# Kernel tuning notes

Measured on AMD Instinct MI355X. Metric: run time of the kernel, lower is better.

The kernel has to match this reference:

```python
import jax, jax.numpy as jnp
import numpy as np

D_EMB = 128
N_CLASSES = 10
ITEM_DIM = 64


def _mlp(x, w1, b1, w2, b2):
    # torch nn.GELU default is exact (erf) gelu
    return jax.nn.gelu(x @ w1 + b1, approximate=False) @ w2 + b2


def sparsemax(z, axis=-1):
    """Euclidean projection of logits onto the probability simplex (sparsemax)."""
    n = z.shape[axis]
    z_sorted = -jnp.sort(-z, axis=axis)                      # descending
    ks = jnp.arange(1, n + 1, dtype=z.dtype)
    csum = jnp.cumsum(z_sorted, axis=axis)
    support = (1.0 + ks * z_sorted) > csum                   # broadcast over last axis
    k_z = jnp.sum(support, axis=axis, keepdims=True)         # support size
    csum_k = jnp.take_along_axis(csum, k_z.astype(jnp.int32) - 1, axis=axis)
    tau = (csum_k - 1.0) / k_z.astype(z.dtype)
    return jnp.maximum(z - tau, 0.0)


def setup_inputs() -> dict:
    key = jax.random.key(0)
    ks = jax.random.split(key, 22)
    d = D_EMB

    def lin(k, fan_in, fan_out):
        lim = (1.0 / fan_in) ** 0.5
        kw, kb = jax.random.split(k)
        w = jax.random.uniform(kw, (fan_in, fan_out), jnp.float32, -lim, lim)
        b = jax.random.uniform(kb, (fan_out,), jnp.float32, -lim, lim)
        return w, b

    wx1, bx1 = lin(ks[0], ITEM_DIM, d)
    wx2, bx2 = lin(ks[1], d, d)
    wq1, bq1 = lin(ks[2], 1, d)
    wq2, bq2 = lin(ks[3], d, d)
    wqp, bqp = lin(ks[4], d, d)
    wkp, bkp = lin(ks[5], d, d)
    wvp, bvp = lin(ks[6], d, d)
    wp1, bp1 = lin(ks[7], d, d)
    wp2, bp2 = lin(ks[8], d, N_CLASSES)

    x_items = jax.random.normal(ks[9], (32, 16384, ITEM_DIM), jnp.float32)
    x_query = jax.random.normal(ks[10], (32, 1), jnp.float32)
    return {
        "x_items": x_items, "x_query": x_query,
        "wx1": wx1, "bx1": bx1, "wx2": wx2, "bx2": bx2,
        "wq1": wq1, "bq1": bq1, "wq2": wq2, "bq2": bq2,
        "wqp": wqp, "bqp": bqp, "wkp": wkp, "bkp": bkp,
        "wvp": wvp, "bvp": bvp, "wp1": wp1, "bp1": bp1,
        "wp2": wp2, "bp2": bp2,
    }


def reference(x_items, x_query, wx1, bx1, wx2, bx2, wq1, bq1, wq2, bq2,
              wqp, bqp, wkp, bkp, wvp, bvp, wp1, bp1, wp2, bp2):
    # x_items: [B, N, item_dim]; x_query: [B, 1] -> unsqueeze(-1) -> [B, 1, 1]
    h_items = _mlp(x_items, wx1, bx1, wx2, bx2)              # [B, N, d]
    h_query = _mlp(x_query[..., None], wq1, bq1, wq2, bq2)   # [B, 1, d]
    q = h_query @ wqp + bqp                                   # [B, 1, d]
    k = h_items @ wkp + bkp                                   # [B, N, d]
    v = h_items @ wvp + bvp                                   # [B, N, d]
    scale = k.shape[-1] ** -0.5
    scores = jnp.einsum('bqd,bnd->bqn', q, k) * scale         # [B, 1, N]
    attn = sparsemax(scores, axis=-1)                         # simplex mapping
    z = jnp.einsum('bqn,bnd->bqd', attn, v)[:, 0]             # squeeze(1) -> [B, d]
    return _mlp(z, wp1, bp1, wp2, bp2)                        # [B, n_classes]
```

## Files before the change

### kernel.cpp

```cpp
#include <hip/hip_runtime.h>
#include <hip/hip_bf16.h>
#include <cstdint>

#define BATCH 32
#define NITEMS 16384
#define DEMB 128
#define IDIM 64

typedef short short8 __attribute__((ext_vector_type(8)));
typedef float f32x4 __attribute__((ext_vector_type(4)));

__device__ inline unsigned short f2bf(float f) {
    union { float f; unsigned int u; } v; v.f = f;
    unsigned int u = v.u;
    unsigned int r = (u + 0x7FFFu + ((u >> 16) & 1u)) >> 16;
    return (unsigned short)r;
}
__device__ inline float bf2f(unsigned short h) {
    union { unsigned int u; float f; } v; v.u = ((unsigned int)h) << 16;
    return v.f;
}

__device__ inline float gelu_f(float x) {
    float y = fabsf(x) * 0.70710678118654752f;
    float t = __builtin_amdgcn_rcpf(fmaf(0.3275911f, y, 1.0f));
    float p = fmaf(0.5307027145f, t, -0.7265760135f);
    p = fmaf(p, t, 0.7107068705f);
    p = fmaf(p, t, -0.142248368f);
    p = fmaf(p, t, 0.127414796f);
    p = p * t;
    float e = __builtin_amdgcn_exp2f(x * x * -0.72134752044448171f);
    float q = p * e;
    float phi = (x > 0.f) ? (1.0f - q) : q;
    return x * phi;
}

__global__ __launch_bounds__(128) void k0_prep(
    const float* __restrict__ xq, const float* __restrict__ wq1, const float* __restrict__ bq1,
    const float* __restrict__ wq2, const float* __restrict__ bq2,
    const float* __restrict__ wqp, const float* __restrict__ bqp,
    const float* __restrict__ wkp,
    const float* __restrict__ wx1, const float* __restrict__ wx2,
    float* __restrict__ r_out, unsigned short* __restrict__ w1h, unsigned short* __restrict__ w1l) {
    __shared__ float buf1[128], buf2[128], buf3[128], buf4[128];
    int t = threadIdx.x;
    int blk = blockIdx.x;
    if (blk < BATCH) {
        int b = blk;
        float xqv = xq[b];
        buf1[t] = gelu_f(fmaf(xqv, wq1[t], bq1[t]));
        __syncthreads();
        float acc = bq2[t];
        for (int j = 0; j < 128; j++) acc = fmaf(buf1[j], wq2[j * 128 + t], acc);
        buf2[t] = acc;
        __syncthreads();
        acc = bqp[t];
        for (int j = 0; j < 128; j++) acc = fmaf(buf2[j], wqp[j * 128 + t], acc);
        buf3[t] = acc;
        __syncthreads();
        acc = 0.f;
        for (int i = 0; i < 128; i++) acc = fmaf(wkp[t * 128 + i], buf3[i], acc);
        buf4[t] = acc * 0.08838834764831845f;
        __syncthreads();
        acc = 0.f;
        for (int i = 0; i < 128; i++) acc = fmaf(wx2[t * 128 + i], buf4[i], acc);
        r_out[b * 128 + t] = acc;
    } else {
        for (int idx = t; idx < 64 * 128; idx += 128) {
            int k = idx >> 7, n = idx & 127;
            float v = wx1[idx];
            unsigned short hi = f2bf(v);
            float lo = v - bf2f(hi);
            w1h[n * 64 + k] = hi;
            w1l[n * 64 + k] = f2bf(lo);
        }
    }
}

__global__ __launch_bounds__(256) void k1_items(
    const float* __restrict__ x, const unsigned short* __restrict__ w1h,
    const unsigned short* __restrict__ w1l, const float* __restrict__ bx1,
    const float* __restrict__ r_in, float* __restrict__ scores) {
    __shared__ alignas(16) unsigned short lxh[64 * 72];
    __shared__ alignas(16) unsigned short lxl[64 * 72];
    __shared__ float red[4][64];
    int tid = threadIdx.x;
    int wave = tid >> 6, lane = tid & 63;
    int quad = lane >> 4, l15 = lane & 15;
    int tile = blockIdx.x;
    long item0 = (long)tile * 64;
    int b = tile >> 8;

    short8 wh[2][2], wl[2][2];
    for (int s = 0; s < 2; s++)
        for (int mt = 0; mt < 2; mt++) {
            int off = (wave * 32 + mt * 16 + l15) * 64 + s * 32 + quad * 8;
            wh[s][mt] = *(const short8*)(w1h + off);
            wl[s][mt] = *(const short8*)(w1l + off);
        }
    float bias8[2][4], rv8[2][4];
    for (int mt = 0; mt < 2; mt++)
        for (int rr = 0; rr < 4; rr++) {
            int row = wave * 32 + mt * 16 + quad * 4 + rr;
            bias8[mt][rr] = bx1[row];
            rv8[mt][rr] = r_in[b * 128 + row];
        }

    const float* xg = x + item0 * 64;
    for (int p = 0; p < 4; p++) {
        int idx = tid + p * 256;
        int row = idx >> 4, c4 = (idx & 15) * 4;
        float4 v = *(const float4*)(xg + row * 64 + c4);
        unsigned int ux = __float_as_uint(v.x), uy = __float_as_uint(v.y);
        unsigned int uz = __float_as_uint(v.z), uw = __float_as_uint(v.w);
        unsigned int hi01 = __builtin_amdgcn_perm(uy, ux, 0x07060302u);
        unsigned int hi23 = __builtin_amdgcn_perm(uw, uz, 0x07060302u);
        float lx = v.x - __uint_as_float(ux & 0xFFFF0000u);
        float ly = v.y - __uint_as_float(uy & 0xFFFF0000u);
        float lz = v.z - __uint_as_float(uz & 0xFFFF0000u);
        float lw = v.w - __uint_as_float(uw & 0xFFFF0000u);
        unsigned int lo01 = __builtin_amdgcn_perm(__float_as_uint(ly), __float_as_uint(lx), 0x07060302u);
        unsigned int lo23 = __builtin_amdgcn_perm(__float_as_uint(lw), __float_as_uint(lz), 0x07060302u);
        *(uint2*)(lxh + row * 72 + c4) = make_uint2(hi01, hi23);
        *(uint2*)(lxl + row * 72 + c4) = make_uint2(lo01, lo23);
    }
    __syncthreads();

    f32x4 acc[2][4];
    for (int mt = 0; mt < 2; mt++)
        for (int nt = 0; nt < 4; nt++) {
            f32x4 bi = {bias8[mt][0], bias8[mt][1], bias8[mt][2], bias8[mt][3]};
            acc[mt][nt] = bi;
        }

    for (int s = 0; s < 2; s++) {
        int koff = s * 32 + quad * 8;
        short8 xh[4], xl[4];
        for (int nt = 0; nt < 4; nt++) {
            int rb = (nt * 16 + l15) * 72 + koff;
            xh[nt] = *(const short8*)(lxh + rb);
            xl[nt] = *(const short8*)(lxl + rb);
        }
        for (int mt = 0; mt < 2; mt++)
            for (int nt = 0; nt < 4; nt++) {
                acc[mt][nt] = __builtin_amdgcn_mfma_f32_16x16x32_bf16(wh[s][mt], xl[nt], acc[mt][nt], 0, 0, 0);
                acc[mt][nt] = __builtin_amdgcn_mfma_f32_16x16x32_bf16(wl[s][mt], xh[nt], acc[mt][nt], 0, 0, 0);
                acc[mt][nt] = __builtin_amdgcn_mfma_f32_16x16x32_bf16(wh[s][mt], xh[nt], acc[mt][nt], 0, 0, 0);
            }
    }

    float pr[4] = {0.f, 0.f, 0.f, 0.f};
    for (int mt = 0; mt < 2; mt++)
        for (int nt = 0; nt < 4; nt++)
            for (int rr = 0; rr < 4; rr++) {
                float g = gelu_f(acc[mt][nt][rr]);
                pr[nt] = fmaf(g, rv8[mt][rr], pr[nt]);
            }
    for (int nt = 0; nt < 4; nt++) {
        pr[nt] += __shfl_xor(pr[nt], 16);
        pr[nt] += __shfl_xor(pr[nt], 32);
    }
    if (quad == 0)
        for (int nt = 0; nt < 4; nt++)
            red[wave][nt * 16 + l15] = pr[nt];
    __syncthreads();
    if (tid < 64)
        scores[item0 + tid] = red[0][tid] + red[1][tid] + red[2][tid] + red[3][tid];
}

__global__ __launch_bounds__(1024) void k2_tau(const float* __restrict__ scores,
                                               float* __restrict__ tau_out,
                                               float* __restrict__ u) {
    __shared__ float la[2][16], lc[2][16];
    int b = blockIdx.x, t = threadIdx.x;
    int wid = t >> 6, lane = t & 63;
    const float* s = scores + (size_t)b * NITEMS;
    float z[16];
    for (int i = 0; i < 16; i++) z[i] = s[t + i * 1024];
    float sm = 0.f;
    for (int i = 0; i < 16; i++) sm += z[i];
    for (int off = 32; off; off >>= 1) sm += __shfl_xor(sm, off);
    if (lane == 0) la[1][wid] = sm;
    __syncthreads();
    float tot = 0.f;
    for (int i = 0; i < 16; i++) tot += la[1][i];
    float tau = (tot - 1.0f) * (1.0f / 16384.0f);
    for (int it = 0; it < 20; it++) {
        int pb = it & 1;
        float ls = 0.f, ct = 0.f;
        for (int i = 0; i < 16; i++) {
            bool a = z[i] > tau;
            ls += a ? z[i] : 0.f;
            ct += a ? 1.f : 0.f;
        }
        for (int off = 32; off; off >>= 1) {
            ls += __shfl_xor(ls, off);
            ct += __shfl_xor(ct, off);
        }
        if (lane == 0) { la[pb][wid] = ls; lc[pb][wid] = ct; }
        __syncthreads();
        float tls = 0.f, tct = 0.f;
        for (int i = 0; i < 16; i++) { tls += la[pb][i]; tct += lc[pb][i]; }
        tau = (tls - 1.0f) / tct;
    }
    if (t == 0) tau_out[b] = tau;
    if (t < 128) u[b * 128 + t] = 0.f;
}

__global__ __launch_bounds__(256) void k3_support(
    const float* __restrict__ scores, const float* __restrict__ tau_in,
    const float* __restrict__ x,
    const float* __restrict__ wx1, const float* __restrict__ bx1,
    const float* __restrict__ wx2, const float* __restrict__ bx2,
    float* __restrict__ u) {
    __shared__ float red[4][128];
    int blk = blockIdx.x;
    int b = blk >> 5;
    int sub = blk & 31;
    int wave = threadIdx.x >> 6, lane = threadIdx.x & 63;
    int wslot = sub * 4 + wave;
    int base = wslot * 128;
    float tau = tau_in[b];
    int t0 = lane, t1 = lane + 64;
    float bb0 = bx1[t0], bb1 = bx1[t1];
    float cc0 = bx2[t0], cc1 = bx2[t1];
    float u0 = 0.f, u1 = 0.f;
    const float* srow = scores + (size_t)b * NITEMS + base;
    for (int half = 0; half < 2; half++) {
        float sv = srow[half * 64 + lane] - tau;
        unsigned long long mask = __ballot(sv > 0.f);
        while (mask) {
            int src = __ffsll((long long)mask) - 1;
            mask &= mask - 1;
            float wgt = __shfl(sv, src);
            int item = base + half * 64 + src;
            const float* xr = x + ((size_t)b * NITEMS + item) * 64;
            float xv = xr[lane];
            float p0 = bb0, p1 = bb1;
            for (int k = 0; k < 64; k++) {
                float xk = __shfl(xv, k);
                p0 = fmaf(xk, wx1[k * 128 + t0], p0);
                p1 = fmaf(xk, wx1[k * 128 + t1], p1);
            }
            float h0 = gelu_f(p0), h1 = gelu_f(p1);
            float a0 = cc0, a1 = cc1;
            for (int j = 0; j < 64; j++) {
                float hj = __shfl(h0, j);
                a0 = fmaf(hj, wx2[j * 128 + t0], a0);
                a1 = fmaf(hj, wx2[j * 128 + t1], a1);
            }
            for (int j = 0; j < 64; j++) {
                float hj = __shfl(h1, j);
                a0 = fmaf(hj, wx2[(j + 64) * 128 + t0], a0);
                a1 = fmaf(hj, wx2[(j + 64) * 128 + t1], a1);
            }
            u0 = fmaf(wgt, a0, u0);
            u1 = fmaf(wgt, a1, u1);
        }
    }
    red[wave][t0] = u0;
    red[wave][t1] = u1;
    __syncthreads();
    if (threadIdx.x < 128) {
        float s = red[0][threadIdx.x] + red[1][threadIdx.x] +
                  red[2][threadIdx.x] + red[3][threadIdx.x];
        atomicAdd(&u[b * 128 + threadIdx.x], s);
    }
}

__global__ __launch_bounds__(128) void k4_head(
    const float* __restrict__ u, const float* __restrict__ wvp, const float* __restrict__ bvp,
    const float* __restrict__ wp1, const float* __restrict__ bp1,
    const float* __restrict__ wp2, const float* __restrict__ bp2,
    float* __restrict__ out) {
    __shared__ float ub[128], zb[128], tb[128];
    int b = blockIdx.x, t = threadIdx.x;
    ub[t] = u[b * 128 + t];
    __syncthreads();
    float z = bvp[t];
    for (int j = 0; j < 128; j++) z = fmaf(ub[j], wvp[j * 128 + t], z);
    zb[t] = z;
    __syncthreads();
    float h = bp1[t];
    for (int j = 0; j < 128; j++) h = fmaf(zb[j], wp1[j * 128 + t], h);
    tb[t] = gelu_f(h);
    __syncthreads();
    if (t < 10) {
        float o = bp2[t];
        for (int j = 0; j < 128; j++) o = fmaf(tb[j], wp2[j * 10 + t], o);
        out[b * 10 + t] = o;
    }
}

extern "C" void kernel_launch(void* const* d_in, const int* in_sizes, int n_in,
                              void* d_out, int out_size, void* d_ws, size_t ws_size,
                              hipStream_t stream) {
    const float* x_items = (const float*)d_in[0];
    const float* x_query = (const float*)d_in[1];
    const float* wx1 = (const float*)d_in[2];
    const float* bx1 = (const float*)d_in[3];
    const float* wx2 = (const float*)d_in[4];
    const float* bx2 = (const float*)d_in[5];
    const float* wq1 = (const float*)d_in[6];
    const float* bq1 = (const float*)d_in[7];
    const float* wq2 = (const float*)d_in[8];
    const float* bq2 = (const float*)d_in[9];
    const float* wqp = (const float*)d_in[10];
    const float* bqp = (const float*)d_in[11];
    const float* wkp = (const float*)d_in[12];
    const float* wvp = (const float*)d_in[14];
    const float* bvp = (const float*)d_in[15];
    const float* wp1 = (const float*)d_in[16];
    const float* bp1 = (const float*)d_in[17];
    const float* wp2 = (const float*)d_in[18];
    const float* bp2 = (const float*)d_in[19];
    float* out = (float*)d_out;

    char* ws = (char*)d_ws;
    float* r_buf        = (float*)(ws);
    unsigned short* w1h = (unsigned short*)(ws + 16384);
    unsigned short* w1l = (unsigned short*)(ws + 32768);
    float* scores       = (float*)(ws + 49152);
    float* tau          = (float*)(ws + 49152 + 2097152);
    float* u            = (float*)(ws + 49152 + 2097152 + 256);

    k0_prep<<<33, 128, 0, stream>>>(x_query, wq1, bq1, wq2, bq2, wqp, bqp, wkp,
                                    wx1, wx2, r_buf, w1h, w1l);
    k1_items<<<(BATCH * NITEMS) / 64, 256, 0, stream>>>(x_items, w1h, w1l, bx1, r_buf, scores);
    k2_tau<<<BATCH, 1024, 0, stream>>>(scores, tau, u);
    k3_support<<<BATCH * 32, 256, 0, stream>>>(scores, tau, x_items, wx1, bx1, wx2, bx2, u);
    k4_head<<<BATCH, 128, 0, stream>>>(u, wvp, bvp, wp1, bp1, wp2, bp2, out);
}
```

Baseline: 329.6 us.

## Fuse head MLP into support kernel via last-block counter; early-exit tau iteration

The head kernel is folded into the support kernel. Each batch has a per-batch atomic counter, and the last of its 32 blocks to finish computes the value projection and output MLP, which removes one kernel launch. The tau fixed-point iteration now starts from a very low threshold and exits as soon as tau stops changing, replacing the fixed 20 iterations and the initial mean pass. This adds fences, an extra atomic and a data-dependent loop bound, and starting from a lower tau may need more iterations to converge.

```diff
diff --git a/kernel.cpp b/kernel.cpp
--- a/kernel.cpp
+++ b/kernel.cpp
@@ -170,22 +170,16 @@
 
 __global__ __launch_bounds__(1024) void k2_tau(const float* __restrict__ scores,
                                                float* __restrict__ tau_out,
-                                               float* __restrict__ u) {
+                                               float* __restrict__ u,
+                                               int* __restrict__ ctr) {
     __shared__ float la[2][16], lc[2][16];
     int b = blockIdx.x, t = threadIdx.x;
     int wid = t >> 6, lane = t & 63;
     const float* s = scores + (size_t)b * NITEMS;
     float z[16];
     for (int i = 0; i < 16; i++) z[i] = s[t + i * 1024];
-    float sm = 0.f;
-    for (int i = 0; i < 16; i++) sm += z[i];
-    for (int off = 32; off; off >>= 1) sm += __shfl_xor(sm, off);
-    if (lane == 0) la[1][wid] = sm;
-    __syncthreads();
-    float tot = 0.f;
-    for (int i = 0; i < 16; i++) tot += la[1][i];
-    float tau = (tot - 1.0f) * (1.0f / 16384.0f);
-    for (int it = 0; it < 20; it++) {
+    float tau = -1e30f;
+    for (int it = 0; it < 21; it++) {
         int pb = it & 1;
         float ls = 0.f, ct = 0.f;
         for (int i = 0; i < 16; i++) {
@@ -201,9 +195,11 @@
         __syncthreads();
         float tls = 0.f, tct = 0.f;
         for (int i = 0; i < 16; i++) { tls += la[pb][i]; tct += lc[pb][i]; }
-        tau = (tls - 1.0f) / tct;
-    }
-    if (t == 0) tau_out[b] = tau;
+        float ntau = (tls - 1.0f) / tct;
+        if (ntau == tau) break;
+        tau = ntau;
+    }
+    if (t == 0) { tau_out[b] = tau; ctr[b] = 0; }
     if (t < 128) u[b * 128 + t] = 0.f;
 }
 
@@ -212,8 +208,13 @@
     const float* __restrict__ x,
     const float* __restrict__ wx1, const float* __restrict__ bx1,
     const float* __restrict__ wx2, const float* __restrict__ bx2,
-    float* __restrict__ u) {
+    float* __restrict__ u, int* __restrict__ ctr,
+    const float* __restrict__ wvp, const float* __restrict__ bvp,
+    const float* __restrict__ wp1, const float* __restrict__ bp1,
+    const float* __restrict__ wp2, const float* __restrict__ bp2,
+    float* __restrict__ out) {
     __shared__ float red[4][128];
+    __shared__ int lastFlag;
     int blk = blockIdx.x;
     int b = blk >> 5;
     int sub = blk & 31;
@@ -266,24 +267,33 @@
                   red[2][threadIdx.x] + red[3][threadIdx.x];
         atomicAdd(&u[b * 128 + threadIdx.x], s);
     }
-}
-
-__global__ __launch_bounds__(128) void k4_head(
-    const float* __restrict__ u, const float* __restrict__ wvp, const float* __restrict__ bvp,
-    const float* __restrict__ wp1, const float* __restrict__ bp1,
-    const float* __restrict__ wp2, const float* __restrict__ bp2,
-    float* __restrict__ out) {
+    __threadfence();
+    __syncthreads();
+    if (threadIdx.x == 0) {
+        int prev = __hip_atomic_fetch_add(&ctr[b], 1, __ATOMIC_ACQ_REL,
+                                          __HIP_MEMORY_SCOPE_AGENT);
+        lastFlag = (prev == 31);
+    }
+    __syncthreads();
+    if (!lastFlag) return;
+
     __shared__ float ub[128], zb[128], tb[128];
-    int b = blockIdx.x, t = threadIdx.x;
-    ub[t] = u[b * 128 + t];
-    __syncthreads();
-    float z = bvp[t];
-    for (int j = 0; j < 128; j++) z = fmaf(ub[j], wvp[j * 128 + t], z);
-    zb[t] = z;
-    __syncthreads();
-    float h = bp1[t];
-    for (int j = 0; j < 128; j++) h = fmaf(zb[j], wp1[j * 128 + t], h);
-    tb[t] = gelu_f(h);
+    int t = threadIdx.x;
+    if (t < 128)
+        ub[t] = __hip_atomic_load(&u[b * 128 + t], __ATOMIC_RELAXED,
+                                  __HIP_MEMORY_SCOPE_AGENT);
+    __syncthreads();
+    if (t < 128) {
+        float zv = bvp[t];
+        for (int j = 0; j < 128; j++) zv = fmaf(ub[j], wvp[j * 128 + t], zv);
+        zb[t] = zv;
+    }
+    __syncthreads();
+    if (t < 128) {
+        float h = bp1[t];
+        for (int j = 0; j < 128; j++) h = fmaf(zb[j], wp1[j * 128 + t], h);
+        tb[t] = gelu_f(h);
+    }
     __syncthreads();
     if (t < 10) {
         float o = bp2[t];
@@ -323,11 +333,12 @@
     float* scores       = (float*)(ws + 49152);
     float* tau          = (float*)(ws + 49152 + 2097152);
     float* u            = (float*)(ws + 49152 + 2097152 + 256);
+    int*   ctr          = (int*)  (ws + 49152 + 2097152 + 256 + 16384);
 
     k0_prep<<<33, 128, 0, stream>>>(x_query, wq1, bq1, wq2, bq2, wqp, bqp, wkp,
                                     wx1, wx2, r_buf, w1h, w1l);
     k1_items<<<(BATCH * NITEMS) / 64, 256, 0, stream>>>(x_items, w1h, w1l, bx1, r_buf, scores);
-    k2_tau<<<BATCH, 1024, 0, stream>>>(scores, tau, u);
-    k3_support<<<BATCH * 32, 256, 0, stream>>>(scores, tau, x_items, wx1, bx1, wx2, bx2, u);
-    k4_head<<<BATCH, 128, 0, stream>>>(u, wvp, bvp, wp1, bp1, wp2, bp2, out);
-}
+    k2_tau<<<BATCH, 1024, 0, stream>>>(scores, tau, u, ctr);
+    k3_support<<<BATCH * 32, 256, 0, stream>>>(scores, tau, x_items, wx1, bx1, wx2, bx2,
+                                               u, ctr, wvp, bvp, wp1, bp1, wp2, bp2, out);
+}
```

After: 375.1 us. 1.14x slower.
